# Kernel optimization log

Hardware: AMD Instinct MI355X
Metric: run time of the kernel (lower is better)

The kernel has to match this reference:

```python
import jax, jax.numpy as jnp
import numpy as np

B, S, C = 16, 2048, 512
E = S            # embed_dim == seq_len (RMSNorm applied on transposed seq axis)
H = 4 * E        # FFN hidden
LAMBDA_INIT = float(0.8 - 0.6 * np.exp(-0.3 * 1.0))  # layer_index = 1
SCALE = E ** (-0.25)
K = 5            # decomposition moving-average kernel


def rmsnorm(x, w, eps=1e-8):
    return x * jax.lax.rsqrt(jnp.mean(x * x, axis=-1, keepdims=True) + eps) * w


def decompose(a):
    # DLinear-style series decomposition: replicate-padded moving average along seq
    pad = (K - 1) // 2
    ap = jnp.concatenate([jnp.repeat(a[:, :1], pad, axis=1), a, jnp.repeat(a[:, -1:], pad, axis=1)], axis=1)
    n = a.shape[1]
    trend = sum(ap[:, i:i + n] for i in range(K)) / K
    return trend, a - trend


def setup_inputs() -> dict:
    key = jax.random.key(0)
    ks = jax.random.split(key, 12)
    p = lambda i, shape, s=0.02: jax.random.normal(ks[i], shape, jnp.float32) * s
    return {
        "x": jax.random.normal(ks[0], (B, S, C), jnp.float32),
        "ln_attn_w": jnp.ones((E,), jnp.float32),
        "q12_w": p(1, (E, 2 * E)), "q12_b": jnp.zeros((2 * E,), jnp.float32),
        "k12_w": p(2, (E, 2 * E)), "k12_b": jnp.zeros((2 * E,), jnp.float32),
        "v_w": p(3, (E, E)), "v_b": jnp.zeros((E,), jnp.float32),
        "lambda_q1": p(4, (E,), 0.1), "lambda_k1": p(5, (E,), 0.1),
        "lambda_q2": p(6, (E,), 0.1), "lambda_k2": p(7, (E,), 0.1),
        "norm_w": jnp.ones((E,), jnp.float32),
        "ln_ff_w": jnp.ones((E,), jnp.float32),
        "ff_w1": p(8, (E, H)), "ff_b1": jnp.zeros((H,), jnp.float32),
        "ff_w2": p(9, (H, E)), "ff_b2": jnp.zeros((E,), jnp.float32),
    }


def reference(x, ln_attn_w, q12_w, q12_b, k12_w, k12_b, v_w, v_b,
              lambda_q1, lambda_k1, lambda_q2, lambda_k2,
              norm_w, ln_ff_w, ff_w1, ff_b1, ff_w2, ff_b2):
    # pre-attention RMSNorm over the seq axis (via transpose)
    a = jnp.swapaxes(rmsnorm(jnp.swapaxes(x, -1, -2), ln_attn_w), -1, -2)  # [B,S,C]
    trend, seasonal = decompose(a)
    # project seq dim of trend/seasonal (iTransformer style: channels are tokens)
    q = jnp.swapaxes(trend, -1, -2) @ q12_w + q12_b      # [B,C,2S]
    q1, q2 = jnp.split(q, 2, axis=-1)                    # [B,C,S] each
    k = jnp.swapaxes(seasonal, -1, -2) @ k12_w + k12_b   # [B,C,2S]
    k1, k2 = jnp.split(k, 2, axis=-1)                    # [B,C,S]
    v = jnp.swapaxes(a, -1, -2) @ v_w + v_b              # [B,C,S]
    a1 = jnp.einsum('bis,bjs->bij', q1, k1) * SCALE      # [B,C,C]
    a2 = jnp.einsum('bis,bjs->bij', q2, k2) * SCALE      # [B,C,C]
    lam = jnp.exp(jnp.sum(lambda_q1 * lambda_k1)) - jnp.exp(jnp.sum(lambda_q2 * lambda_k2)) + LAMBDA_INIT
    d = jax.nn.softmax(a1, axis=-1) - lam * jax.nn.softmax(a2, axis=-1)
    attn = rmsnorm(d @ v, norm_w) * (1.0 - LAMBDA_INIT)  # [B,C,S]
    x = x + jnp.swapaxes(attn, -1, -2)
    # FFN over the seq axis
    h = rmsnorm(jnp.swapaxes(x, -1, -2), ln_ff_w)        # [B,C,S]
    ff = jax.nn.gelu(h @ ff_w1 + ff_b1, approximate=False) @ ff_w2 + ff_b2
    return x + jnp.swapaxes(ff, -1, -2)
```

## Files before the change

kernel.cpp:

```cpp
#include <hip/hip_runtime.h>
#include <hip/hip_bf16.h>

#define B_ 16
#define S_ 2048
#define C_ 512
#define H_ 8192

#define LAMBDA_INIT_F 0.3555090675909693f
#define ONE_M_LI_F    0.6444909324090307f
#define SCALE_F       0.14865088937534013f

using bf16x8 = __attribute__((ext_vector_type(8))) short;
using f32x4  = __attribute__((ext_vector_type(4))) float;

__device__ __forceinline__ float b2f(ushort u) {
  union { unsigned u; float f; } x; x.u = ((unsigned)u) << 16; return x.f;
}
__device__ __forceinline__ ushort f2b(float f) {
  union { float f; unsigned u; } x; x.f = f;
  unsigned r = x.u + 0x7fffu + ((x.u >> 16) & 1u);
  return (ushort)(r >> 16);
}

__device__ __forceinline__ void load_lds16(const void* g, void* s) {
  __builtin_amdgcn_global_load_lds((const __attribute__((address_space(1))) void*)g,
                                   (__attribute__((address_space(3))) void*)s,
                                   16, 0, 0);
}

__device__ __forceinline__ float block_sum(float v, float* red) {
#pragma unroll
  for (int o = 32; o > 0; o >>= 1) v += __shfl_down(v, o, 64);
  __syncthreads();
  if ((threadIdx.x & 63) == 0) red[threadIdx.x >> 6] = v;
  __syncthreads();
  return red[0] + red[1] + red[2] + red[3];
}
__device__ __forceinline__ float block_max(float v, float* red) {
#pragma unroll
  for (int o = 32; o > 0; o >>= 1) v = fmaxf(v, __shfl_down(v, o, 64));
  __syncthreads();
  if ((threadIdx.x & 63) == 0) red[threadIdx.x >> 6] = v;
  __syncthreads();
  return fmaxf(fmaxf(red[0], red[1]), fmaxf(red[2], red[3]));
}

template <int EPI>
__global__ __launch_bounds__(256, 2) void gemm_nt(
    const ushort* __restrict__ Aall, const ushort* __restrict__ Ball,
    void* __restrict__ Call, const float* __restrict__ bias,
    int K, int lda, int ldb, int ldc,
    long sA, long sB, long sC, long sA2, long sB2, float alpha)
{
  __shared__ ushort lA[4096];
  __shared__ ushort lB[4096];
  const int t = threadIdx.x;
  const int m0 = blockIdx.x * 128, n0 = blockIdx.y * 128;
  const int zb = blockIdx.z & 15, zh = blockIdx.z >> 4;
  const ushort* A  = Aall + (size_t)zb * sA + (size_t)zh * sA2;
  const ushort* Bt = Ball + (size_t)zb * sB + (size_t)zh * sB2;
  const int lane = t & 63;
  const int wave = t >> 6;
  const int wm = (wave >> 1) * 64, wn = (wave & 1) * 64;
  const int fr = lane & 15, kh = lane >> 4;
  f32x4 acc[4][4] = {};
  const int srow = t >> 2;
  const int scol = (t & 3) * 8;
  const size_t ar0 = (size_t)(m0 + srow) * lda + scol;
  const size_t ar1 = (size_t)(m0 + 64 + srow) * lda + scol;
  const size_t br0 = (size_t)(n0 + srow) * ldb + scol;
  const size_t br1 = (size_t)(n0 + 64 + srow) * ldb + scol;
  const int wbase = wave * 512;

  for (int k0 = 0; k0 < K; k0 += 32) {
    __syncthreads();
    load_lds16(A + ar0 + k0,  &lA[wbase]);
    load_lds16(A + ar1 + k0,  &lA[2048 + wbase]);
    load_lds16(Bt + br0 + k0, &lB[wbase]);
    load_lds16(Bt + br1 + k0, &lB[2048 + wbase]);
    __syncthreads();
    bf16x8 af[4], bg[4];
#pragma unroll
    for (int i = 0; i < 4; ++i)
      af[i] = *(const bf16x8*)&lA[(wm + i * 16 + fr) * 32 + kh * 8];
#pragma unroll
    for (int j = 0; j < 4; ++j)
      bg[j] = *(const bf16x8*)&lB[(wn + j * 16 + fr) * 32 + kh * 8];
#pragma unroll
    for (int i = 0; i < 4; ++i)
#pragma unroll
      for (int j = 0; j < 4; ++j)
        acc[i][j] = __builtin_amdgcn_mfma_f32_16x16x32_bf16(af[i], bg[j], acc[i][j], 0, 0, 0);
  }

  const int r0 = kh * 4;
  if constexpr (EPI == 0) {
    float* C = (float*)Call + (size_t)blockIdx.z * sC;
#pragma unroll
    for (int i = 0; i < 4; ++i)
#pragma unroll
      for (int j = 0; j < 4; ++j) {
        const int gr = m0 + wm + i * 16 + r0;
        const int gc = n0 + wn + j * 16 + fr;
#pragma unroll
        for (int r = 0; r < 4; ++r)
          C[(size_t)(gr + r) * ldc + gc] = acc[i][j][r] * alpha;
      }
  } else {
    ushort* C = (ushort*)Call + (size_t)blockIdx.z * sC;
#pragma unroll
    for (int i = 0; i < 4; ++i)
#pragma unroll
      for (int j = 0; j < 4; ++j) {
        const int gr = m0 + wm + i * 16 + r0;
        const int gc = n0 + wn + j * 16 + fr;
        const float bb = (EPI == 3) ? 0.f : bias[gc];
#pragma unroll
        for (int r = 0; r < 4; ++r) {
          float v = acc[i][j][r] + bb;
          if constexpr (EPI == 3) v = acc[i][j][r] * alpha;
          if constexpr (EPI == 2) v = 0.5f * v * (1.f + erff(v * 0.7071067811865475f));
          C[(size_t)(gr + r) * ldc + gc] = f2b(v);
        }
      }
  }
}


__global__ __launch_bounds__(256) void k_rms_part(const float* __restrict__ x, float* __restrict__ part) {
  const int c = blockIdx.x * 256 + threadIdx.x;
  const int sl = blockIdx.y;
  const int b = blockIdx.z;
  const float* p = x + (size_t)b * S_ * C_ + c;
  const int s0 = sl * 256;
  float s = 0.f;
  for (int i = 0; i < 256; ++i) { float v = p[(size_t)(s0 + i) * C_]; s += v * v; }
  part[((size_t)b * C_ + c) * 8 + sl] = s;
}
__global__ __launch_bounds__(256) void k_rms_fin(const float* __restrict__ part, float* __restrict__ rms1) {
  const int i = blockIdx.x * 256 + threadIdx.x;
  const float* p = part + (size_t)i * 8;
  float s = 0.f;
#pragma unroll
  for (int j = 0; j < 8; ++j) s += p[j];
  rms1[i] = rsqrtf(s * (1.f / S_) + 1e-8f);
}

__global__ __launch_bounds__(256) void k_trans_norm(const float* __restrict__ x, const float* __restrict__ rms1,
                                                    const float* __restrict__ w,
                                                    ushort* __restrict__ aT, ushort* __restrict__ xT) {
  __shared__ float tile[32][33];
  const int s0 = blockIdx.x * 32, c0 = blockIdx.y * 32, b = blockIdx.z;
  const int tx = threadIdx.x, ty = threadIdx.y;
  const float* xb = x + (size_t)b * S_ * C_;
#pragma unroll
  for (int r = 0; r < 4; ++r) {
    const int s = ty + 8 * r;
    tile[s][tx] = xb[(size_t)(s0 + s) * C_ + c0 + tx];
  }
  __syncthreads();
#pragma unroll
  for (int r = 0; r < 4; ++r) {
    const int c = ty + 8 * r;
    const float v = tile[tx][c];
    const float rm = rms1[b * C_ + c0 + c];
    const size_t o = ((size_t)b * C_ + c0 + c) * S_ + s0 + tx;
    xT[o] = f2b(v);
    aT[o] = f2b(v * rm * w[s0 + tx]);
  }
}

__global__ __launch_bounds__(256) void k_wtrans(const float* __restrict__ W, ushort* __restrict__ WT,
                                                int Kd, int Ndstride, int n_base) {
  __shared__ float tile[32][33];
  const int k0 = blockIdx.x * 32, n0 = blockIdx.y * 32;
  const int tx = threadIdx.x, ty = threadIdx.y;
#pragma unroll
  for (int r = 0; r < 4; ++r) {
    const int k = ty + 8 * r;
    tile[k][tx] = W[(size_t)(k0 + k) * Ndstride + n_base + n0 + tx];
  }
  __syncthreads();
#pragma unroll
  for (int r = 0; r < 4; ++r) {
    const int n = ty + 8 * r;
    WT[(size_t)(n0 + n) * Kd + k0 + tx] = f2b(tile[tx][n]);
  }
}

__global__ __launch_bounds__(256) void k_bt(const ushort* __restrict__ in, ushort* __restrict__ out, int R, int CL) {
  __shared__ ushort tile[32][33];
  const int r0 = blockIdx.x * 32, c0 = blockIdx.y * 32;
  const size_t zb = (size_t)blockIdx.z * R * CL;
  const int tx = threadIdx.x, ty = threadIdx.y;
#pragma unroll
  for (int r = 0; r < 4; ++r) {
    const int rr = ty + 8 * r;
    tile[rr][tx] = in[zb + (size_t)(r0 + rr) * CL + c0 + tx];
  }
  __syncthreads();
#pragma unroll
  for (int r = 0; r < 4; ++r) {
    const int cc = ty + 8 * r;
    out[zb + (size_t)(c0 + cc) * R + r0 + tx] = tile[tx][cc];
  }
}

__device__ __forceinline__ float trend5(const ushort* p, int s) {
  float sum = 0.f;
#pragma unroll
  for (int d = -2; d <= 2; ++d) {
    int ss = s + d; ss = ss < 0 ? 0 : (ss > S_ - 1 ? S_ - 1 : ss);
    sum += b2f(p[ss]);
  }
  return sum * 0.2f;
}
__global__ __launch_bounds__(256) void k_dtrend(const ushort* __restrict__ aT, ushort* __restrict__ trT) {
  const size_t i = (size_t)blockIdx.x * 256 + threadIdx.x;
  const int s = (int)(i & (S_ - 1));
  trT[i] = f2b(trend5(aT + (i - s), s));
}
__global__ __launch_bounds__(256) void k_dseason(const ushort* __restrict__ aT, ushort* __restrict__ seT) {
  const size_t i = (size_t)blockIdx.x * 256 + threadIdx.x;
  const int s = (int)(i & (S_ - 1));
  const ushort* p = aT + (i - s);
  seT[i] = f2b(b2f(p[s]) - trend5(p, s));
}

__global__ __launch_bounds__(256) void k_lambda(const float* __restrict__ lq1, const float* __restrict__ lk1,
                                                const float* __restrict__ lq2, const float* __restrict__ lk2,
                                                float* __restrict__ lam) {
  __shared__ float r1[4], r2[4];
  const int t = threadIdx.x;
  float s1 = 0.f, s2 = 0.f;
  for (int i = t; i < S_; i += 256) { s1 += lq1[i] * lk1[i]; s2 += lq2[i] * lk2[i]; }
#pragma unroll
  for (int o = 32; o > 0; o >>= 1) { s1 += __shfl_down(s1, o, 64); s2 += __shfl_down(s2, o, 64); }
  if ((t & 63) == 0) { r1[t >> 6] = s1; r2[t >> 6] = s2; }
  __syncthreads();
  if (t == 0) {
    const float a = r1[0] + r1[1] + r1[2] + r1[3];
    const float b = r2[0] + r2[1] + r2[2] + r2[3];
    *lam = expf(a) - expf(b) + LAMBDA_INIT_F;
  }
}

__global__ __launch_bounds__(256) void k_softmax(const float* __restrict__ a1, const float* __restrict__ a2,
                                                 const float* __restrict__ lamp, ushort* __restrict__ dm) {
  __shared__ float red[4];
  const size_t row = blockIdx.x;
  const float* p1 = a1 + row * 512;
  const float* p2 = a2 + row * 512;
  const int t = threadIdx.x;
  const float v1a = p1[t], v1b = p1[t + 256];
  const float v2a = p2[t], v2b = p2[t + 256];
  const float m1 = block_max(fmaxf(v1a, v1b), red);
  const float m2 = block_max(fmaxf(v2a, v2b), red);
  const float e1a = expf(v1a - m1), e1b = expf(v1b - m1);
  const float e2a = expf(v2a - m2), e2b = expf(v2b - m2);
  const float s1 = block_sum(e1a + e1b, red);
  const float s2 = block_sum(e2a + e2b, red);
  const float i1 = 1.f / s1, i2 = (*lamp) / s2;
  ushort* o = dm + row * 512;
  o[t]       = f2b(e1a * i1 - e2a * i2);
  o[t + 256] = f2b(e1b * i1 - e2b * i2);
}

__global__ __launch_bounds__(256) void k_postattn(const ushort* __restrict__ P, const ushort* __restrict__ xT,
                                                  const float* __restrict__ norm_w, const float* __restrict__ ln_ff_w,
                                                  ushort* __restrict__ attn, ushort* __restrict__ h) {
  __shared__ float red[4];
  const size_t row = blockIdx.x;
  const ushort* p = P + row * S_;
  const int t = threadIdx.x;
  float v[8]; float ss = 0.f;
#pragma unroll
  for (int i = 0; i < 8; ++i) { v[i] = b2f(p[t + 256 * i]); ss += v[i] * v[i]; }
  ss = block_sum(ss, red);
  const float inv = rsqrtf(ss * (1.f / S_) + 1e-8f);
  const ushort* xr = xT + row * S_;
  ushort* ar = attn + row * S_;
  float x2[8]; float ss2 = 0.f;
#pragma unroll
  for (int i = 0; i < 8; ++i) {
    const int s = t + 256 * i;
    const float at = v[i] * inv * norm_w[s] * ONE_M_LI_F;
    ar[s] = f2b(at);
    const float xx = b2f(xr[s]) + at;
    x2[i] = xx; ss2 += xx * xx;
  }
  ss2 = block_sum(ss2, red);
  const float inv2 = rsqrtf(ss2 * (1.f / S_) + 1e-8f);
  ushort* hr = h + row * S_;
#pragma unroll
  for (int i = 0; i < 8; ++i) { const int s = t + 256 * i; hr[s] = f2b(x2[i] * inv2 * ln_ff_w[s]); }
}

__global__ __launch_bounds__(256) void k_final(const float* __restrict__ x, const ushort* __restrict__ attn,
                                               const ushort* __restrict__ ffo, float* __restrict__ out) {
  __shared__ float tile[32][33];
  const int s0 = blockIdx.x * 32, c0 = blockIdx.y * 32, b = blockIdx.z;
  const int tx = threadIdx.x, ty = threadIdx.y;
#pragma unroll
  for (int r = 0; r < 4; ++r) {
    const int c = ty + 8 * r;
    const size_t idx = ((size_t)b * C_ + c0 + c) * S_ + s0 + tx;
    tile[c][tx] = b2f(attn[idx]) + b2f(ffo[idx]);
  }
  __syncthreads();
#pragma unroll
  for (int r = 0; r < 4; ++r) {
    const int s = ty + 8 * r;
    const size_t o = ((size_t)b * S_ + s0 + s) * C_ + c0 + tx;
    out[o] = x[o] + tile[tx][s];
  }
}

__global__ void k_probe(float* out, float v) { out[0] = v; }

extern "C" void kernel_launch(void* const* d_in, const int* in_sizes, int n_in,
                              void* d_out, int out_size, void* d_ws, size_t ws_size,
                              hipStream_t stream) {
  const float* x       = (const float*)d_in[0];
  const float* ln_attn = (const float*)d_in[1];
  const float* q12_w   = (const float*)d_in[2];
  const float* q12_b   = (const float*)d_in[3];
  const float* k12_w   = (const float*)d_in[4];
  const float* k12_b   = (const float*)d_in[5];
  const float* v_w     = (const float*)d_in[6];
  const float* v_b     = (const float*)d_in[7];
  const float* lq1     = (const float*)d_in[8];
  const float* lk1     = (const float*)d_in[9];
  const float* lq2     = (const float*)d_in[10];
  const float* lk2     = (const float*)d_in[11];
  const float* norm_w  = (const float*)d_in[12];
  const float* ln_ff   = (const float*)d_in[13];
  const float* ff_w1   = (const float*)d_in[14];
  const float* ff_b1   = (const float*)d_in[15];
  const float* ff_w2   = (const float*)d_in[16];
  const float* ff_b2   = (const float*)d_in[17];
  float* out = (float*)d_out;

  if (ws_size < 184844544ull) {
    k_probe<<<1, 1, 0, stream>>>(out, (float)(ws_size >> 20));
    return;
  }

  char* ws = (char*)d_ws;
  ushort* slotA = (ushort*)(ws + 0);
  ushort* slotB = (ushort*)(ws + 33554432);
  ushort* slotC = (ushort*)(ws + 67108864);
  ushort* slotD = (ushort*)(ws + 100663296);
  ushort* slotE = (ushort*)(ws + 134217728);
  ushort* slotF = (ushort*)(ws + 167772160);
  float*  part  = (float*) (ws + 184549376);
  float*  rms1  = (float*) (ws + 184811520);
  float*  lamp  = (float*) (ws + 184844288);

  ushort* aT   = slotA;
  ushort* xT   = slotE;
  ushort* Vm   = slotB;
  ushort* VT   = slotD;
  ushort* trT  = slotB;
  ushort* seT  = slotC;
  ushort* K12  = slotA;
  float*  scr  = (float*)slotC;
  ushort* Pm   = slotB;
  ushort* attn = slotC;
  ushort* hbuf = slotA;
  ushort* ff1T = slotB;
  ushort* ff2T = slotD;
  ushort* ffo  = slotE;
  ushort* wsl  = slotF;
  ushort* dmat = slotF;
  ushort* Qm   = (ushort*)d_out;
  ushort* H1c  = (ushort*)d_out;

  const dim3 blk256(256), blkT(32, 8);

  k_rms_part<<<dim3(2, 8, B_), blk256, 0, stream>>>(x, part);
  k_rms_fin<<<dim3(32), blk256, 0, stream>>>(part, rms1);
  k_trans_norm<<<dim3(64, 16, B_), blkT, 0, stream>>>(x, rms1, ln_attn, aT, xT);

  k_wtrans<<<dim3(64, 64), blkT, 0, stream>>>(v_w, wsl, 2048, 2048, 0);
  gemm_nt<1><<<dim3(64, 16), blk256, 0, stream>>>(aT, wsl, Vm, v_b, 2048, 2048, 2048, 2048,
                                                  0, 0, 0, 0, 0, 1.f);
  k_bt<<<dim3(16, 64, B_), blkT, 0, stream>>>(Vm, VT, 512, 2048);

  k_dtrend<<<dim3(65536), blk256, 0, stream>>>(aT, trT);
  k_wtrans<<<dim3(64, 128), blkT, 0, stream>>>(q12_w, wsl, 2048, 4096, 0);
  gemm_nt<1><<<dim3(64, 32), blk256, 0, stream>>>(trT, wsl, Qm, q12_b, 2048, 2048, 2048, 4096,
                                                  0, 0, 0, 0, 0, 1.f);

  k_dseason<<<dim3(65536), blk256, 0, stream>>>(aT, seT);
  k_lambda<<<dim3(1), blk256, 0, stream>>>(lq1, lk1, lq2, lk2, lamp);
  k_wtrans<<<dim3(64, 128), blkT, 0, stream>>>(k12_w, wsl, 2048, 4096, 0);
  gemm_nt<1><<<dim3(64, 32), blk256, 0, stream>>>(seT, wsl, K12, k12_b, 2048, 2048, 2048, 4096,
                                                  0, 0, 0, 0, 0, 1.f);

  gemm_nt<0><<<dim3(4, 4, 32), blk256, 0, stream>>>(Qm, K12, scr, nullptr, 2048, 4096, 4096, 512,
                                                    512L * 4096, 512L * 4096, 512L * 512,
                                                    2048L, 2048L, SCALE_F);

  k_softmax<<<dim3(8192), blk256, 0, stream>>>(scr, scr + 4194304, lamp, dmat);
  gemm_nt<3><<<dim3(4, 16, B_), blk256, 0, stream>>>(dmat, VT, Pm, nullptr, 512, 512, 512, 2048,
                                                     512L * 512, 2048L * 512, 512L * 2048,
                                                     0, 0, 1.f);

  k_postattn<<<dim3(8192), blk256, 0, stream>>>(Pm, xT, norm_w, ln_ff, attn, hbuf);

  k_wtrans<<<dim3(64, 256), blkT, 0, stream>>>(ff_w1, ff1T, 2048, 8192, 0);
  k_wtrans<<<dim3(256, 64), blkT, 0, stream>>>(ff_w2, ff2T, 8192, 2048, 0);

  for (int c = 0; c < 2; ++c) {
    const size_t moff = (size_t)c * 4096 * 2048;
    gemm_nt<2><<<dim3(32, 64), blk256, 0, stream>>>(hbuf + moff, ff1T, H1c, ff_b1,
                                                    2048, 2048, 2048, 8192, 0, 0, 0, 0, 0, 1.f);
    gemm_nt<1><<<dim3(32, 16), blk256, 0, stream>>>(H1c, ff2T, ffo + moff, ff_b2,
                                                    8192, 8192, 8192, 2048, 0, 0, 0, 0, 0, 1.f);
  }

  k_final<<<dim3(64, 16, B_), blkT, 0, stream>>>(x, attn, ffo, out);
}
```

Measured before the change: 1.447 ms.

## Add 256x256 swizzled MFMA GEMM and split FFN along hidden dim

Adds a 512-thread GEMM with 256x256 tiles, XOR-swizzled LDS, double-buffered direct global-to-LDS loads, an L2-friendly block swizzle and priority hints. It replaces the projection and FFN GEMMs, which raises arithmetic intensity per tile and reduces the number of launches. The FFN is now split along the hidden dimension instead of the rows. The second FFN GEMM accumulates into the bf16 output and adds the attention residual in its epilogue, so the final kernel reads one input instead of two. In exchange there is an extra bf16 rounding of the partial FFN sum, only one block per CU, and a much heavier 128 KB LDS footprint.

```diff
diff --git a/kernel.cpp b/kernel.cpp
--- a/kernel.cpp
+++ b/kernel.cpp
@@ -28,28 +28,150 @@
                                    16, 0, 0);
 }
 
-__device__ __forceinline__ float block_sum(float v, float* red) {
-#pragma unroll
-  for (int o = 32; o > 0; o >>= 1) v += __shfl_down(v, o, 64);
-  __syncthreads();
-  if ((threadIdx.x & 63) == 0) red[threadIdx.x >> 6] = v;
-  __syncthreads();
-  return red[0] + red[1] + red[2] + red[3];
-}
-__device__ __forceinline__ float block_max(float v, float* red) {
-#pragma unroll
-  for (int o = 32; o > 0; o >>= 1) v = fmaxf(v, __shfl_down(v, o, 64));
-  __syncthreads();
-  if ((threadIdx.x & 63) == 0) red[threadIdx.x >> 6] = v;
-  __syncthreads();
-  return fmaxf(fmaxf(red[0], red[1]), fmaxf(red[2], red[3]));
+#define WAITV4() do { asm volatile("s_waitcnt vmcnt(4)" ::: "memory"); __builtin_amdgcn_sched_barrier(0); } while (0)
+#define WAITV0() do { asm volatile("s_waitcnt vmcnt(0)" ::: "memory"); __builtin_amdgcn_sched_barrier(0); } while (0)
+#define WAITL0() do { asm volatile("s_waitcnt lgkmcnt(0)" ::: "memory"); __builtin_amdgcn_sched_barrier(0); } while (0)
+#define BAR()    __builtin_amdgcn_s_barrier()
+
+template <int EPI>
+__global__ __launch_bounds__(512, 1) void gemm256(
+    const ushort* __restrict__ A, const ushort* __restrict__ Bt,
+    ushort* __restrict__ C, const float* __restrict__ bias,
+    const ushort* __restrict__ addm,
+    int K, int lda, int ldb, int ldc)
+{
+  __shared__ ushort lds[65536];
+  const int t = threadIdx.x, w = t >> 6, lane = t & 63;
+  const int fr = lane & 15, khl = lane >> 4;
+  const int wr = w >> 2, wc = w & 3;
+
+  const int gx = gridDim.x;
+  const int id = blockIdx.y * gx + blockIdx.x;
+  const int nwg = gx * gridDim.y;
+  const int swz = (id & 7) * (nwg >> 3) + (id >> 3);
+  const int m0 = (swz % gx) * 256, n0 = (swz / gx) * 256;
+
+  const int sl    = (t & 7) ^ ((t >> 3) & 7);
+  const int rbase = ((t >> 3) << 1) + (sl >> 2);
+  const int khs   = sl & 3;
+  const size_t aoff = (size_t)(m0 + rbase) * lda + khs * 8;
+  const size_t boff = (size_t)(n0 + rbase) * ldb + khs * 8;
+  const size_t jstA = (size_t)128 * lda, jstB = (size_t)128 * ldb;
+
+  int ao[8], bo[4];
+#pragma unroll
+  for (int m = 0; m < 8; ++m) {
+    const int row = wr * 128 + m * 16 + fr, dr = row >> 1;
+    const int so = (((row & 1) << 2) + khl) ^ (dr & 7);
+    ao[m] = dr * 64 + so * 8;
+  }
+#pragma unroll
+  for (int n = 0; n < 4; ++n) {
+    const int row = wc * 64 + n * 16 + fr, dr = row >> 1;
+    const int so = (((row & 1) << 2) + khl) ^ (dr & 7);
+    bo[n] = 16384 + dr * 64 + so * 8;
+  }
+
+  f32x4 acc[8][4] = {};
+  const int NT = K >> 6;
+
+#define STAGE_A(ch, nb, k1) do { const ushort* s_ = A + aoff + (k1) + (ch) * 32; \
+    ushort* d_ = &lds[(nb) + (ch) * 8192 + w * 512]; \
+    load_lds16(s_, d_); load_lds16(s_ + jstA, d_ + 4096); } while (0)
+#define STAGE_B(ch, nb, k1) do { const ushort* s_ = Bt + boff + (k1) + (ch) * 32; \
+    ushort* d_ = &lds[(nb) + 16384 + (ch) * 8192 + w * 512]; \
+    load_lds16(s_, d_); load_lds16(s_ + jstB, d_ + 4096); } while (0)
+#define LDA(cb, ch, m) (*(const bf16x8*)&lds[(cb) + (ch) * 8192 + ao[m]])
+#define LDB(cb, ch, n) (*(const bf16x8*)&lds[(cb) + (ch) * 8192 + bo[n]])
+#define MFMA8(mlo, nf, bg) _Pragma("unroll") for (int m_ = 0; m_ < 8; ++m_) \
+    acc[m_][nf] = __builtin_amdgcn_mfma_f32_16x16x32_bf16(af[m_], bg, acc[m_][nf], 0, 0, 0)
+
+  STAGE_A(0, 0, 0); STAGE_B(0, 0, 0); STAGE_A(1, 0, 0); STAGE_B(1, 0, 0);
+  WAITV4(); BAR();
+
+  bf16x8 af[8];
+  for (int kt = 0; kt < NT - 1; ++kt) {
+    const int cb = (kt & 1) << 15, nb = cb ^ 32768;
+    const int k1 = (kt + 1) << 6;
+    bf16x8 b0, b1;
+#pragma unroll
+    for (int m = 0; m < 8; ++m) af[m] = LDA(cb, 0, m);
+    b0 = LDB(cb, 0, 0); b1 = LDB(cb, 0, 1);
+    STAGE_A(0, nb, k1);
+    BAR(); WAITL0();
+    __builtin_amdgcn_s_setprio(1); MFMA8(0, 0, b0); MFMA8(0, 1, b1); __builtin_amdgcn_s_setprio(0);
+    BAR();
+    b0 = LDB(cb, 0, 2); b1 = LDB(cb, 0, 3);
+    STAGE_B(0, nb, k1);
+    WAITV4(); BAR(); WAITL0();
+    __builtin_amdgcn_s_setprio(1); MFMA8(0, 2, b0); MFMA8(0, 3, b1); __builtin_amdgcn_s_setprio(0);
+    BAR();
+#pragma unroll
+    for (int m = 0; m < 8; ++m) af[m] = LDA(cb, 1, m);
+    b0 = LDB(cb, 1, 0); b1 = LDB(cb, 1, 1);
+    STAGE_A(1, nb, k1);
+    BAR(); WAITL0();
+    __builtin_amdgcn_s_setprio(1); MFMA8(1, 0, b0); MFMA8(1, 1, b1); __builtin_amdgcn_s_setprio(0);
+    BAR();
+    b0 = LDB(cb, 1, 2); b1 = LDB(cb, 1, 3);
+    STAGE_B(1, nb, k1);
+    WAITV4(); BAR(); WAITL0();
+    __builtin_amdgcn_s_setprio(1); MFMA8(1, 2, b0); MFMA8(1, 3, b1); __builtin_amdgcn_s_setprio(0);
+    BAR();
+  }
+  {
+    const int cb = ((NT - 1) & 1) << 15;
+    bf16x8 b0, b1;
+#pragma unroll
+    for (int m = 0; m < 8; ++m) af[m] = LDA(cb, 0, m);
+    b0 = LDB(cb, 0, 0); b1 = LDB(cb, 0, 1);
+    BAR(); WAITL0();
+    MFMA8(0, 0, b0); MFMA8(0, 1, b1);
+    BAR();
+    b0 = LDB(cb, 0, 2); b1 = LDB(cb, 0, 3);
+    WAITV0(); BAR(); WAITL0();
+    MFMA8(0, 2, b0); MFMA8(0, 3, b1);
+    BAR();
+#pragma unroll
+    for (int m = 0; m < 8; ++m) af[m] = LDA(cb, 1, m);
+    b0 = LDB(cb, 1, 0); b1 = LDB(cb, 1, 1);
+    BAR(); WAITL0();
+    MFMA8(1, 0, b0); MFMA8(1, 1, b1);
+    BAR();
+    b0 = LDB(cb, 1, 2); b1 = LDB(cb, 1, 3);
+    BAR(); WAITL0();
+    MFMA8(1, 2, b0); MFMA8(1, 3, b1);
+  }
+#undef STAGE_A
+#undef STAGE_B
+#undef LDA
+#undef LDB
+#undef MFMA8
+
+  const int r0 = khl * 4;
+#pragma unroll
+  for (int m = 0; m < 8; ++m)
+#pragma unroll
+    for (int nf = 0; nf < 4; ++nf) {
+      const int gr = m0 + wr * 128 + m * 16 + r0;
+      const int gc = n0 + wc * 64 + nf * 16 + fr;
+      const float bb = (EPI == 3) ? 0.f : bias[gc];
+#pragma unroll
+      for (int r = 0; r < 4; ++r) {
+        const size_t idx = (size_t)(gr + r) * ldc + gc;
+        float v = acc[m][nf][r];
+        if constexpr (EPI == 1) v += bb;
+        if constexpr (EPI == 2) { v += bb; v = 0.5f * v * (1.f + erff(v * 0.7071067811865475f)); }
+        if constexpr (EPI == 4) v += bb + b2f(addm[idx]) + b2f(C[idx]);
+        C[idx] = f2b(v);
+      }
+    }
 }
 
 template <int EPI>
 __global__ __launch_bounds__(256, 2) void gemm_nt(
     const ushort* __restrict__ Aall, const ushort* __restrict__ Ball,
-    void* __restrict__ Call, const float* __restrict__ bias,
-    int K, int lda, int ldb, int ldc,
+    void* __restrict__ Call, int K, int lda, int ldb, int ldc,
     long sA, long sB, long sC, long sA2, long sB2, float alpha)
 {
   __shared__ ushort lA[4096];
@@ -114,18 +236,29 @@
       for (int j = 0; j < 4; ++j) {
         const int gr = m0 + wm + i * 16 + r0;
         const int gc = n0 + wn + j * 16 + fr;
-        const float bb = (EPI == 3) ? 0.f : bias[gc];
-#pragma unroll
-        for (int r = 0; r < 4; ++r) {
-          float v = acc[i][j][r] + bb;
-          if constexpr (EPI == 3) v = acc[i][j][r] * alpha;
-          if constexpr (EPI == 2) v = 0.5f * v * (1.f + erff(v * 0.7071067811865475f));
-          C[(size_t)(gr + r) * ldc + gc] = f2b(v);
-        }
+#pragma unroll
+        for (int r = 0; r < 4; ++r)
+          C[(size_t)(gr + r) * ldc + gc] = f2b(acc[i][j][r] * alpha);
       }
   }
 }
 
+__device__ __forceinline__ float block_sum(float v, float* red) {
+#pragma unroll
+  for (int o = 32; o > 0; o >>= 1) v += __shfl_down(v, o, 64);
+  __syncthreads();
+  if ((threadIdx.x & 63) == 0) red[threadIdx.x >> 6] = v;
+  __syncthreads();
+  return red[0] + red[1] + red[2] + red[3];
+}
+__device__ __forceinline__ float block_max(float v, float* red) {
+#pragma unroll
+  for (int o = 32; o > 0; o >>= 1) v = fmaxf(v, __shfl_down(v, o, 64));
+  __syncthreads();
+  if ((threadIdx.x & 63) == 0) red[threadIdx.x >> 6] = v;
+  __syncthreads();
+  return fmaxf(fmaxf(red[0], red[1]), fmaxf(red[2], red[3]));
+}
 
 __global__ __launch_bounds__(256) void k_rms_part(const float* __restrict__ x, float* __restrict__ part) {
   const int c = blockIdx.x * 256 + threadIdx.x;
@@ -296,16 +429,15 @@
   for (int i = 0; i < 8; ++i) { const int s = t + 256 * i; hr[s] = f2b(x2[i] * inv2 * ln_ff_w[s]); }
 }
 
-__global__ __launch_bounds__(256) void k_final(const float* __restrict__ x, const ushort* __restrict__ attn,
-                                               const ushort* __restrict__ ffo, float* __restrict__ out) {
+__global__ __launch_bounds__(256) void k_final2(const float* __restrict__ x, const ushort* __restrict__ sumT,
+                                                float* __restrict__ out) {
   __shared__ float tile[32][33];
   const int s0 = blockIdx.x * 32, c0 = blockIdx.y * 32, b = blockIdx.z;
   const int tx = threadIdx.x, ty = threadIdx.y;
 #pragma unroll
   for (int r = 0; r < 4; ++r) {
     const int c = ty + 8 * r;
-    const size_t idx = ((size_t)b * C_ + c0 + c) * S_ + s0 + tx;
-    tile[c][tx] = b2f(attn[idx]) + b2f(ffo[idx]);
+    tile[c][tx] = b2f(sumT[((size_t)b * C_ + c0 + c) * S_ + s0 + tx]);
   }
   __syncthreads();
 #pragma unroll
@@ -374,36 +506,33 @@
   ushort* wsl  = slotF;
   ushort* dmat = slotF;
   ushort* Qm   = (ushort*)d_out;
-  ushort* H1c  = (ushort*)d_out;
-
-  const dim3 blk256(256), blkT(32, 8);
+  ushort* H1   = (ushort*)d_out;
+
+  const dim3 blk256(256), blk512(512), blkT(32, 8);
 
   k_rms_part<<<dim3(2, 8, B_), blk256, 0, stream>>>(x, part);
   k_rms_fin<<<dim3(32), blk256, 0, stream>>>(part, rms1);
   k_trans_norm<<<dim3(64, 16, B_), blkT, 0, stream>>>(x, rms1, ln_attn, aT, xT);
 
   k_wtrans<<<dim3(64, 64), blkT, 0, stream>>>(v_w, wsl, 2048, 2048, 0);
-  gemm_nt<1><<<dim3(64, 16), blk256, 0, stream>>>(aT, wsl, Vm, v_b, 2048, 2048, 2048, 2048,
-                                                  0, 0, 0, 0, 0, 1.f);
+  gemm256<1><<<dim3(32, 8), blk512, 0, stream>>>(aT, wsl, Vm, v_b, nullptr, 2048, 2048, 2048, 2048);
   k_bt<<<dim3(16, 64, B_), blkT, 0, stream>>>(Vm, VT, 512, 2048);
 
   k_dtrend<<<dim3(65536), blk256, 0, stream>>>(aT, trT);
   k_wtrans<<<dim3(64, 128), blkT, 0, stream>>>(q12_w, wsl, 2048, 4096, 0);
-  gemm_nt<1><<<dim3(64, 32), blk256, 0, stream>>>(trT, wsl, Qm, q12_b, 2048, 2048, 2048, 4096,
-                                                  0, 0, 0, 0, 0, 1.f);
+  gemm256<1><<<dim3(32, 16), blk512, 0, stream>>>(trT, wsl, Qm, q12_b, nullptr, 2048, 2048, 2048, 4096);
 
   k_dseason<<<dim3(65536), blk256, 0, stream>>>(aT, seT);
   k_lambda<<<dim3(1), blk256, 0, stream>>>(lq1, lk1, lq2, lk2, lamp);
   k_wtrans<<<dim3(64, 128), blkT, 0, stream>>>(k12_w, wsl, 2048, 4096, 0);
-  gemm_nt<1><<<dim3(64, 32), blk256, 0, stream>>>(seT, wsl, K12, k12_b, 2048, 2048, 2048, 4096,
-                                                  0, 0, 0, 0, 0, 1.f);
-
-  gemm_nt<0><<<dim3(4, 4, 32), blk256, 0, stream>>>(Qm, K12, scr, nullptr, 2048, 4096, 4096, 512,
+  gemm256<1><<<dim3(32, 16), blk512, 0, stream>>>(seT, wsl, K12, k12_b, nullptr, 2048, 2048, 2048, 4096);
+
+  gemm_nt<0><<<dim3(4, 4, 32), blk256, 0, stream>>>(Qm, K12, scr, 2048, 4096, 4096, 512,
                                                     512L * 4096, 512L * 4096, 512L * 512,
                                                     2048L, 2048L, SCALE_F);
 
   k_softmax<<<dim3(8192), blk256, 0, stream>>>(scr, scr + 4194304, lamp, dmat);
-  gemm_nt<3><<<dim3(4, 16, B_), blk256, 0, stream>>>(dmat, VT, Pm, nullptr, 512, 512, 512, 2048,
+  gemm_nt<3><<<dim3(4, 16, B_), blk256, 0, stream>>>(dmat, VT, Pm, 512, 512, 512, 2048,
                                                      512L * 512, 2048L * 512, 512L * 2048,
                                                      0, 0, 1.f);
 
@@ -412,13 +541,14 @@
   k_wtrans<<<dim3(64, 256), blkT, 0, stream>>>(ff_w1, ff1T, 2048, 8192, 0);
   k_wtrans<<<dim3(256, 64), blkT, 0, stream>>>(ff_w2, ff2T, 8192, 2048, 0);
 
-  for (int c = 0; c < 2; ++c) {
-    const size_t moff = (size_t)c * 4096 * 2048;
-    gemm_nt<2><<<dim3(32, 64), blk256, 0, stream>>>(hbuf + moff, ff1T, H1c, ff_b1,
-                                                    2048, 2048, 2048, 8192, 0, 0, 0, 0, 0, 1.f);
-    gemm_nt<1><<<dim3(32, 16), blk256, 0, stream>>>(H1c, ff2T, ffo + moff, ff_b2,
-                                                    8192, 8192, 8192, 2048, 0, 0, 0, 0, 0, 1.f);
-  }
-
-  k_final<<<dim3(64, 16, B_), blkT, 0, stream>>>(x, attn, ffo, out);
-}
+  gemm256<2><<<dim3(32, 16), blk512, 0, stream>>>(hbuf, ff1T, H1, ff_b1, nullptr,
+                                                  2048, 2048, 2048, 4096);
+  gemm256<3><<<dim3(32, 8), blk512, 0, stream>>>(H1, ff2T, ffo, nullptr, nullptr,
+                                                 4096, 4096, 8192, 2048);
+  gemm256<2><<<dim3(32, 16), blk512, 0, stream>>>(hbuf, ff1T + (size_t)4096 * 2048, H1,
+                                                  ff_b1 + 4096, nullptr, 2048, 2048, 2048, 4096);
+  gemm256<4><<<dim3(32, 8), blk512, 0, stream>>>(H1, ff2T + 4096, ffo, ff_b2, attn,
+                                                 4096, 4096, 8192, 2048);
+
+  k_final2<<<dim3(64, 16, B_), blkT, 0, stream>>>(x, ffo, out);
+}
```

New measurement: 1.329 ms. -8.2%, faster.
